# Kernel tuning notes

Hardware: AMD Instinct MI355X
Metric: run time of the kernel (lower is better)

## Reference

```python
import jax, jax.numpy as jnp
import numpy as np

EPS = 1e-5

def setup_inputs() -> dict:
    key = jax.random.key(0)
    pos = jax.random.normal(key, (8192, 3), dtype=jnp.float32)
    return {"pos": pos}

def reference(pos) -> jnp.ndarray:
    # diff[i, j] = pos[i] - pos[j]  -> [N, N, 3]
    diff = pos[:, None, :] - pos[None, :, :]
    # dist[i, j] = ||diff[i, j]|| + eps  -> [N, N]
    dist = jnp.linalg.norm(diff, axis=2) + EPS
    # force[i, j] = diff / dist^3, then sum over j  -> [N, 3]
    force = diff / (dist ** 3)[:, :, None]
    return force.sum(axis=1)
```

## Files before the change

kernel.cpp:

```cpp
#include <hip/hip_runtime.h>

#define NPTS   8192
#define BLOCK  256
#define CHUNKS 64
#define JT     (NPTS / CHUNKS)

__global__ __launch_bounds__(BLOCK) void nbody_force(
    const float* __restrict__ pos, float* __restrict__ out)
{
    const int tid = threadIdx.x;
    const int i   = blockIdx.x * BLOCK + tid;
    const int j0  = blockIdx.y * JT;

    const float xi = pos[i * 3 + 0];
    const float yi = pos[i * 3 + 1];
    const float zi = pos[i * 3 + 2];

    float fx = 0.0f, fy = 0.0f, fz = 0.0f;

#pragma unroll 8
    for (int t = 0; t < JT; ++t) {
        const int j = j0 + t;
        const float xj = pos[j * 3 + 0];
        const float yj = pos[j * 3 + 1];
        const float zj = pos[j * 3 + 2];

        const float dx = xi - xj;
        const float dy = yi - yj;
        const float dz = zi - zj;
        const float r2 = fmaf(dz, dz, fmaf(dy, dy, fmaf(dx, dx, 1e-12f)));
        const float ir  = __builtin_amdgcn_rsqf(r2);
        const float ir3 = ir * ir * ir;
        fx = fmaf(dx, ir3, fx);
        fy = fmaf(dy, ir3, fy);
        fz = fmaf(dz, ir3, fz);
    }

    atomicAdd(&out[i * 3 + 0], fx);
    atomicAdd(&out[i * 3 + 1], fy);
    atomicAdd(&out[i * 3 + 2], fz);
}

extern "C" void kernel_launch(void* const* d_in, const int* in_sizes, int n_in,
                              void* d_out, int out_size, void* d_ws, size_t ws_size,
                              hipStream_t stream)
{
    const float* pos = (const float*)d_in[0];
    float* out = (float*)d_out;

    hipMemsetAsync(d_out, 0, (size_t)out_size * sizeof(float), stream);

    dim3 grid(NPTS / BLOCK, CHUNKS);
    dim3 block(BLOCK);
    nbody_force<<<grid, block, 0, stream>>>(pos, out);
}
```

Before: 31.60 us.

## Replace atomics with workspace partials plus reduce kernel; load positions as float4

The per-chunk atomicAdd accumulation and the memset are replaced by per-chunk partial results written to a workspace, which a second kernel then sums deterministically. The inner loop now loads four j-positions as three float4 vector loads instead of twelve scalar loads. This removes the atomic contention and the memset launch, at the cost of a 6 MB workspace round trip and an extra kernel launch.

```diff
diff --git a/kernel.cpp b/kernel.cpp
--- a/kernel.cpp
+++ b/kernel.cpp
@@ -5,8 +5,8 @@
 #define CHUNKS 64
 #define JT     (NPTS / CHUNKS)
 
-__global__ __launch_bounds__(BLOCK) void nbody_force(
-    const float* __restrict__ pos, float* __restrict__ out)
+__global__ __launch_bounds__(BLOCK) void nbody_partial(
+    const float* __restrict__ pos, float* __restrict__ ws)
 {
     const int tid = threadIdx.x;
     const int i   = blockIdx.x * BLOCK + tid;
@@ -18,27 +18,47 @@
 
     float fx = 0.0f, fy = 0.0f, fz = 0.0f;
 
-#pragma unroll 8
-    for (int t = 0; t < JT; ++t) {
-        const int j = j0 + t;
-        const float xj = pos[j * 3 + 0];
-        const float yj = pos[j * 3 + 1];
-        const float zj = pos[j * 3 + 2];
+    const float4* __restrict__ pos4 = (const float4*)pos;
 
-        const float dx = xi - xj;
-        const float dy = yi - yj;
-        const float dz = zi - zj;
-        const float r2 = fmaf(dz, dz, fmaf(dy, dy, fmaf(dx, dx, 1e-12f)));
-        const float ir  = __builtin_amdgcn_rsqf(r2);
-        const float ir3 = ir * ir * ir;
-        fx = fmaf(dx, ir3, fx);
-        fy = fmaf(dy, ir3, fy);
-        fz = fmaf(dz, ir3, fz);
+#define PAIR(px, py, pz)                                                    \
+    {                                                                       \
+        const float dx = xi - (px);                                         \
+        const float dy = yi - (py);                                         \
+        const float dz = zi - (pz);                                         \
+        const float r2  = fmaf(dz, dz, fmaf(dy, dy, fmaf(dx, dx, 1e-12f))); \
+        const float ir  = __builtin_amdgcn_rsqf(r2);                        \
+        const float ir3 = ir * ir * ir;                                     \
+        fx = fmaf(dx, ir3, fx);                                             \
+        fy = fmaf(dy, ir3, fy);                                             \
+        fz = fmaf(dz, ir3, fz);                                             \
     }
 
-    atomicAdd(&out[i * 3 + 0], fx);
-    atomicAdd(&out[i * 3 + 1], fy);
-    atomicAdd(&out[i * 3 + 2], fz);
+#pragma unroll 4
+    for (int g = 0; g < JT / 4; ++g) {
+        const int base = (j0 / 4 + g) * 3;
+        const float4 a = pos4[base + 0];
+        const float4 b = pos4[base + 1];
+        const float4 c = pos4[base + 2];
+        PAIR(a.x, a.y, a.z);
+        PAIR(a.w, b.x, b.y);
+        PAIR(b.z, b.w, c.x);
+        PAIR(c.y, c.z, c.w);
+    }
+#undef PAIR
+
+    float* o = ws + ((size_t)blockIdx.y * NPTS + i) * 3;
+    o[0] = fx; o[1] = fy; o[2] = fz;
+}
+
+__global__ __launch_bounds__(BLOCK) void nbody_reduce(
+    const float* __restrict__ ws, float* __restrict__ out)
+{
+    const int e = blockIdx.x * BLOCK + threadIdx.x;
+    float s = 0.0f;
+#pragma unroll 16
+    for (int ch = 0; ch < CHUNKS; ++ch)
+        s += ws[(size_t)ch * NPTS * 3 + e];
+    out[e] = s;
 }
 
 extern "C" void kernel_launch(void* const* d_in, const int* in_sizes, int n_in,
@@ -47,10 +67,11 @@
 {
     const float* pos = (const float*)d_in[0];
     float* out = (float*)d_out;
+    float* ws  = (float*)d_ws;
 
-    hipMemsetAsync(d_out, 0, (size_t)out_size * sizeof(float), stream);
+    dim3 grid1(NPTS / BLOCK, CHUNKS);
+    nbody_partial<<<grid1, dim3(BLOCK), 0, stream>>>(pos, ws);
 
-    dim3 grid(NPTS / BLOCK, CHUNKS);
-    dim3 block(BLOCK);
-    nbody_force<<<grid, block, 0, stream>>>(pos, out);
+    dim3 grid2(NPTS * 3 / BLOCK);
+    nbody_reduce<<<grid2, dim3(BLOCK), 0, stream>>>(ws, out);
 }
```

Result: no change. 32.08 us (+1.5%).

## Pack positions to SoA, use packed float2 math, replace atomics with partial-sum reduction

Applied to the files above, without the earlier changes.

Adds a pre-pass that repacks the AoS positions into separate X/Y/Z arrays in workspace. The force kernel then processes two j-points per iteration using 2-wide vector math, so the compiler can emit packed FP32 ops. Each chunk writes its partial sums to workspace instead of issuing atomics, and a third kernel sums the 64 partials with float4 loads. This removes the memset and atomic contention and reduces ALU instruction count, at the cost of two extra kernel launches and extra workspace traffic.

```diff
diff --git a/kernel.cpp b/kernel.cpp
--- a/kernel.cpp
+++ b/kernel.cpp
@@ -1,44 +1,76 @@
 #include <hip/hip_runtime.h>
+
+typedef float v2f __attribute__((ext_vector_type(2)));
 
 #define NPTS   8192
 #define BLOCK  256
 #define CHUNKS 64
 #define JT     (NPTS / CHUNKS)
 
-__global__ __launch_bounds__(BLOCK) void nbody_force(
-    const float* __restrict__ pos, float* __restrict__ out)
+#define WS_POFF (3 * NPTS)
+
+__global__ __launch_bounds__(BLOCK) void soa_pack(
+    const float* __restrict__ pos,
+    float* __restrict__ X, float* __restrict__ Y, float* __restrict__ Z)
+{
+    const int t = blockIdx.x * BLOCK + threadIdx.x;
+    X[t] = pos[t * 3 + 0];
+    Y[t] = pos[t * 3 + 1];
+    Z[t] = pos[t * 3 + 2];
+}
+
+__global__ __launch_bounds__(BLOCK) void nbody_partial(
+    const float* __restrict__ X, const float* __restrict__ Y,
+    const float* __restrict__ Z, float* __restrict__ part)
 {
     const int tid = threadIdx.x;
     const int i   = blockIdx.x * BLOCK + tid;
-    const int j0  = blockIdx.y * JT;
+    const int g0  = blockIdx.y * (JT / 2);
 
-    const float xi = pos[i * 3 + 0];
-    const float yi = pos[i * 3 + 1];
-    const float zi = pos[i * 3 + 2];
+    const float xi = X[i], yi = Y[i], zi = Z[i];
+    const v2f xi2 = {xi, xi}, yi2 = {yi, yi}, zi2 = {zi, zi};
+    const v2f eps2 = {1e-12f, 1e-12f};
+    v2f fx = {0.f, 0.f}, fy = {0.f, 0.f}, fz = {0.f, 0.f};
 
-    float fx = 0.0f, fy = 0.0f, fz = 0.0f;
+    const v2f* __restrict__ X2 = (const v2f*)X;
+    const v2f* __restrict__ Y2 = (const v2f*)Y;
+    const v2f* __restrict__ Z2 = (const v2f*)Z;
 
 #pragma unroll 8
-    for (int t = 0; t < JT; ++t) {
-        const int j = j0 + t;
-        const float xj = pos[j * 3 + 0];
-        const float yj = pos[j * 3 + 1];
-        const float zj = pos[j * 3 + 2];
-
-        const float dx = xi - xj;
-        const float dy = yi - yj;
-        const float dz = zi - zj;
-        const float r2 = fmaf(dz, dz, fmaf(dy, dy, fmaf(dx, dx, 1e-12f)));
-        const float ir  = __builtin_amdgcn_rsqf(r2);
-        const float ir3 = ir * ir * ir;
-        fx = fmaf(dx, ir3, fx);
-        fy = fmaf(dy, ir3, fy);
-        fz = fmaf(dz, ir3, fz);
+    for (int g = 0; g < JT / 2; ++g) {
+        const int u = g0 + g;
+        const v2f dx = xi2 - X2[u];
+        const v2f dy = yi2 - Y2[u];
+        const v2f dz = zi2 - Z2[u];
+        v2f r2 = dx * dx + eps2;
+        r2 = dy * dy + r2;
+        r2 = dz * dz + r2;
+        v2f ir;
+        ir.x = __builtin_amdgcn_rsqf(r2.x);
+        ir.y = __builtin_amdgcn_rsqf(r2.y);
+        const v2f ir3 = (ir * ir) * ir;
+        fx = dx * ir3 + fx;
+        fy = dy * ir3 + fy;
+        fz = dz * ir3 + fz;
     }
 
-    atomicAdd(&out[i * 3 + 0], fx);
-    atomicAdd(&out[i * 3 + 1], fy);
-    atomicAdd(&out[i * 3 + 2], fz);
+    float* o = part + ((size_t)blockIdx.y * NPTS + i) * 3;
+    o[0] = fx.x + fx.y;
+    o[1] = fy.x + fy.y;
+    o[2] = fz.x + fz.y;
+}
+
+__global__ __launch_bounds__(BLOCK) void nbody_reduce(
+    const float4* __restrict__ part, float4* __restrict__ out)
+{
+    const int e = blockIdx.x * BLOCK + threadIdx.x;
+    float4 s = make_float4(0.f, 0.f, 0.f, 0.f);
+#pragma unroll 8
+    for (int ch = 0; ch < CHUNKS; ++ch) {
+        const float4 v = part[(size_t)ch * (NPTS * 3 / 4) + e];
+        s.x += v.x; s.y += v.y; s.z += v.z; s.w += v.w;
+    }
+    out[e] = s;
 }
 
 extern "C" void kernel_launch(void* const* d_in, const int* in_sizes, int n_in,
@@ -46,11 +78,18 @@
                               hipStream_t stream)
 {
     const float* pos = (const float*)d_in[0];
-    float* out = (float*)d_out;
+    float* wsf = (float*)d_ws;
+    float* X = wsf;
+    float* Y = wsf + NPTS;
+    float* Z = wsf + 2 * NPTS;
+    float* part = wsf + WS_POFF;
 
-    hipMemsetAsync(d_out, 0, (size_t)out_size * sizeof(float), stream);
+    soa_pack<<<dim3(NPTS / BLOCK), dim3(BLOCK), 0, stream>>>(pos, X, Y, Z);
 
-    dim3 grid(NPTS / BLOCK, CHUNKS);
-    dim3 block(BLOCK);
-    nbody_force<<<grid, block, 0, stream>>>(pos, out);
+    dim3 grid1(NPTS / BLOCK, CHUNKS);
+    nbody_partial<<<grid1, dim3(BLOCK), 0, stream>>>(X, Y, Z, part);
+
+    dim3 grid2(NPTS * 3 / 4 / BLOCK);
+    nbody_reduce<<<grid2, dim3(BLOCK), 0, stream>>>((const float4*)part,
+                                                    (float4*)d_out);
 }
```

Result: slower. 34.60 us (+9.5%).
